# Optimization experiments

Measured on AMD Instinct MI355X. Metric: run time of the kernel, lower is better.

## Reference

```python
import jax, jax.numpy as jnp
import numpy as np

R = 16      # grid resolution per axis (G = R**3 voxels)
K = 8       # num KNN neighbors per voxel
H = 64      # num_hidden
NB = 2      # num conv blocks
EPS = 1e-5


def _conv3d(x, w, b):
    # x: [B,C,D,H,W], w: [O,I,3,3,3]
    y = jax.lax.conv_general_dilated(
        x, w, window_strides=(1, 1, 1), padding='SAME',
        dimension_numbers=('NCDHW', 'OIDHW', 'NCDHW'))
    return y + b[None, :, None, None, None]


def _bn(x):
    # training-mode BatchNorm3d statistics (no affine), per channel
    m = x.mean(axis=(0, 2, 3, 4), keepdims=True)
    v = x.var(axis=(0, 2, 3, 4), keepdims=True)
    return (x - m) * jax.lax.rsqrt(v + EPS)


def _forward(pos, x, pe_w1, pe_b1, pe_w2, pe_b2, f_w, f_b, up_w, up_b,
             conv_w, conv_b, on_g, on_b, ro_w, ro_b):
    B, N, _ = pos.shape
    # ---- Gridifier: coordinate grid over domain [-1, 1]^3 ----
    g1 = jnp.linspace(-1.0, 1.0, R, dtype=pos.dtype)
    grid = jnp.stack(jnp.meshgrid(g1, g1, g1, indexing='ij'), axis=-1).reshape(-1, 3)  # [G,3]
    # ---- brute-force KNN: points -> grid voxels (per graph) ----
    gn = jnp.sum(grid * grid, axis=-1)          # [G]
    pn = jnp.sum(pos * pos, axis=-1)            # [B,N]
    d = gn[None, :, None] + pn[:, None, :] - 2.0 * jnp.einsum('gc,bnc->bgn', grid, pos)  # [B,G,N]
    idx = jax.lax.top_k(jax.lax.stop_gradient(-d), K)[1]  # [B,G,K] nearest point indices
    b_ix = jnp.arange(B)[:, None, None]
    p_nb = pos[b_ix, idx]                       # [B,G,K,3] neighbor positions
    f_nb = x[b_ix, idx]                         # [B,G,K,Cin] neighbor features
    # ---- BipartiteConv: position-conditioned messages, mean aggregation ----
    rel = p_nb - grid[None, :, None, :]         # relative positions [B,G,K,3]
    pe = jax.nn.gelu(rel @ pe_w1 + pe_b1) @ pe_w2 + pe_b2   # position embed [B,G,K,H]
    msg = pe * (f_nb @ f_w + f_b)               # multiplicative conditioning [B,G,K,H]
    agg = msg.mean(axis=2)                      # [B,G,H]
    h = jax.nn.gelu(agg @ up_w + up_b)          # update net [B,G,H]
    # reshape(B,R,R,R,H).permute(0,4,3,2,1) -> NCDHW
    vol = h.reshape(B, R, R, R, H).transpose(0, 4, 3, 2, 1)  # [B,H,R,R,R]
    # ---- ConvNet3D: residual blocks, maxpool after block 0 ----
    for i in range(NB):
        h1 = jax.nn.relu(_bn(_conv3d(vol, conv_w[i, 0], conv_b[i, 0])))
        h2 = _bn(_conv3d(h1, conv_w[i, 1], conv_b[i, 1]))
        vol = jax.nn.relu(vol + h2)
        if i == 0:
            vol = jax.lax.reduce_window(vol, -jnp.inf, jax.lax.max,
                                        (1, 1, 2, 2, 2), (1, 1, 2, 2, 2), 'VALID')
    out = _bn(vol) * on_g[None, :, None, None, None] + on_b[None, :, None, None, None]
    # ---- mean readout pool + linear head ----
    pooled = out.mean(axis=(2, 3, 4))           # [B,H]
    return pooled @ ro_w + ro_b                 # [B,out_channels]


def setup_inputs() -> dict:
    key = jax.random.key(0)
    ks = jax.random.split(key, 10)
    B, N, Cin, OUT = 4, 4096, 3, 16
    s = 0.05
    return {
        'pos': jax.random.uniform(ks[0], (B, N, 3), jnp.float32, -1.0, 1.0),
        'x': jax.random.normal(ks[1], (B, N, Cin), jnp.float32),
        'pe_w1': jax.random.normal(ks[2], (3, H), jnp.float32) * 0.3,
        'pe_b1': jnp.zeros((H,), jnp.float32),
        'pe_w2': jax.random.normal(ks[3], (H, H), jnp.float32) * s,
        'pe_b2': jnp.zeros((H,), jnp.float32),
        'f_w': jax.random.normal(ks[4], (Cin, H), jnp.float32) * 0.3,
        'f_b': jnp.zeros((H,), jnp.float32),
        'up_w': jax.random.normal(ks[5], (H, H), jnp.float32) * s,
        'up_b': jnp.zeros((H,), jnp.float32),
        'conv_w': jax.random.normal(ks[6], (NB, 2, H, H, 3, 3, 3), jnp.float32) * s,
        'conv_b': jnp.zeros((NB, 2, H), jnp.float32),
        'on_g': jnp.ones((H,), jnp.float32),
        'on_b': jnp.zeros((H,), jnp.float32),
        'ro_w': jax.random.normal(ks[7], (H, OUT), jnp.float32) * s,
        'ro_b': jnp.zeros((OUT,), jnp.float32),
    }


def reference(pos, x, pe_w1, pe_b1, pe_w2, pe_b2, f_w, f_b, up_w, up_b,
              conv_w, conv_b, on_g, on_b, ro_w, ro_b):
    return _forward(pos, x, pe_w1, pe_b1, pe_w2, pe_b2, f_w, f_b, up_w, up_b,
                    conv_w, conv_b, on_g, on_b, ro_w, ro_b)
```

## Files before the change

kernel.cpp:

```cpp
#include <hip/hip_runtime.h>

#define ULL unsigned long long
typedef unsigned short ush;
typedef __attribute__((ext_vector_type(8))) short s8v;
typedef __attribute__((ext_vector_type(4))) float f4v;

#define BB 4
#define NP 4096
#define HH 64
#define EPSF 1e-5f

#define WH_OFF      0u
#define WL_OFF      221184u
#define WT_PER_CONV 110592u
#define IDX_OFF     442368u
#define VOL0_OFF    573440u
#define V0H_OFF     2066432u
#define V0L_OFF     2812928u
#define T1_OFF      3559424u
#define VOL1_OFF    4608000u
#define V1H_OFF     4864000u
#define V1L_OFF     4992000u
#define T3_OFF      5120000u
#define STATS_OFF   5251072u
#define CELLS_OFF   5251968u
#define SPOS_OFF    5268368u
#define MW_OFF      5333904u

#define ZN_V0   373248u
#define ZN_V1   64000u
#define ZN_ST   224u
#define ZN_ALL  (ZN_V0 + ZN_V1 + ZN_ST)

__device__ __forceinline__ ush f2bf(float f) {
  unsigned u = __float_as_uint(f);
  return (ush)((u + 0x7FFFu + ((u >> 16) & 1u)) >> 16);
}
__device__ __forceinline__ float bf2f(ush h) { return __uint_as_float(((unsigned)h) << 16); }

__device__ __forceinline__ float gelu_tanh(float v) {
  float inner = 0.7978845608028654f * (v + 0.044715f * v * v * v);
  return 0.5f * v * (1.0f + tanhf(inner));
}

__device__ __forceinline__ float lin16(int i) {
  return -1.0f + (float)i * (2.0f / 15.0f);
}

__global__ __launch_bounds__(256) void k_prep(const float* __restrict__ cw,
                                              const float* __restrict__ pw2,
                                              const float* __restrict__ upw,
                                              ush* __restrict__ wh,
                                              ush* __restrict__ wl,
                                              ush* __restrict__ mw,
                                              float* __restrict__ ws) {
  unsigned i = blockIdx.x * 256u + threadIdx.x;
  float4 z = make_float4(0.f, 0.f, 0.f, 0.f);
  if (i < ZN_V0) ((float4*)(ws + V0H_OFF))[i] = z;
  else if (i < ZN_V0 + ZN_V1) ((float4*)(ws + V1H_OFF))[i - ZN_V0] = z;
  else if (i < ZN_ALL) ((float4*)(ws + STATS_OFF))[i - ZN_V0 - ZN_V1] = z;
  if (i < 442368u) {
    unsigned conv = i / WT_PER_CONV;
    unsigned r = i - conv * WT_PER_CONV;
    unsigned co = r / 1728u;
    unsigned r2 = r - co * 1728u;
    unsigned ci = r2 / 27u;
    unsigned off = r2 - ci * 27u;
    float w = cw[i];
    ush hi = f2bf(w);
    unsigned dst = conv * WT_PER_CONV + (off * 64u + co) * 64u + ci;
    wh[dst] = hi;
    wl[dst] = f2bf(w - bf2f(hi));
  } else if (i < 450560u) {
    unsigned t = i - 442368u;
    unsigned mat = t >> 12, r = t & 4095u;
    unsigned co = r >> 6, ci = r & 63u;
    const float* src = mat ? upw : pw2;
    float w = src[ci * 64u + co];
    ush hi = f2bf(w);
    mw[mat * 8192u + co * 64u + ci] = hi;
    mw[mat * 8192u + 4096u + co * 64u + ci] = f2bf(w - bf2f(hi));
  }
}

__global__ __launch_bounds__(256) void k_bin(const float* __restrict__ pos,
                                             int* __restrict__ cellStart,
                                             float4* __restrict__ sortedPos) {
  __shared__ int cnt[4096];
  __shared__ int wsum[4];
  int tid = threadIdx.x;
  int b = blockIdx.x;
  const float* pb = pos + b * NP * 3;
  for (int i = tid; i < 4096; i += 256) cnt[i] = 0;
  __syncthreads();
#pragma unroll
  for (int t = 0; t < 16; ++t) {
    int p = t * 256 + tid;
    float px = pb[3 * p], py = pb[3 * p + 1], pz = pb[3 * p + 2];
    int c0 = (int)floorf((px + 1.0f) * 7.5f + 0.5f);
    int c1 = (int)floorf((py + 1.0f) * 7.5f + 0.5f);
    int c2 = (int)floorf((pz + 1.0f) * 7.5f + 0.5f);
    c0 = min(max(c0, 0), 15); c1 = min(max(c1, 0), 15); c2 = min(max(c2, 0), 15);
    atomicAdd(&cnt[(c0 * 16 + c1) * 16 + c2], 1);
  }
  __syncthreads();
  int base = tid * 16;
  int loc[16];
  int run = 0;
#pragma unroll
  for (int j = 0; j < 16; ++j) { loc[j] = run; run += cnt[base + j]; }
  int lane = tid & 63, wv = tid >> 6;
  int inc = run;
  for (int d = 1; d < 64; d <<= 1) {
    int o = __shfl_up(inc, d, 64);
    if (lane >= d) inc += o;
  }
  if (lane == 63) wsum[wv] = inc;
  __syncthreads();
  int woff = 0;
  for (int w = 0; w < wv; ++w) woff += wsum[w];
  int excl = woff + inc - run;
  __syncthreads();
  int stv[16];
#pragma unroll
  for (int j = 0; j < 16; ++j) {
    stv[j] = excl + loc[j];
    cellStart[b * 4097 + base + j] = stv[j];
  }
#pragma unroll
  for (int j = 0; j < 16; ++j) cnt[base + j] = stv[j];
  if (tid == 0) cellStart[b * 4097 + 4096] = NP;
  __syncthreads();
#pragma unroll
  for (int t = 0; t < 16; ++t) {
    int p = t * 256 + tid;
    float px = pb[3 * p], py = pb[3 * p + 1], pz = pb[3 * p + 2];
    int c0 = (int)floorf((px + 1.0f) * 7.5f + 0.5f);
    int c1 = (int)floorf((py + 1.0f) * 7.5f + 0.5f);
    int c2 = (int)floorf((pz + 1.0f) * 7.5f + 0.5f);
    c0 = min(max(c0, 0), 15); c1 = min(max(c1, 0), 15); c2 = min(max(c2, 0), 15);
    int slot = atomicAdd(&cnt[(c0 * 16 + c1) * 16 + c2], 1);
    sortedPos[b * 4096 + slot] = make_float4(px, py, pz, __int_as_float(p));
  }
}

__device__ __forceinline__ void ins8(ULL* kk, ULL key) {
  if (key < kk[7]) {
    kk[7] = key;
#pragma unroll
    for (int q = 7; q >= 1; --q) {
      ULL a = kk[q - 1], c = kk[q];
      bool sw = c < a;
      kk[q - 1] = sw ? c : a;
      kk[q] = sw ? a : c;
    }
  }
}
__device__ __forceinline__ ULL merge32(ULL* kk, int sub) {
  ULL win = ~0ULL;
#pragma unroll
  for (int r = 0; r < 8; ++r) {
    ULL m = kk[0];
#pragma unroll
    for (int s = 1; s < 32; s <<= 1) {
      ULL o = __shfl_xor(m, s, 64);
      m = (o < m) ? o : m;
    }
    if (kk[0] == m) {
#pragma unroll
      for (int q = 0; q < 7; ++q) kk[q] = kk[q + 1];
      kk[7] = ~0ULL;
    }
    if (sub == r) win = m;
  }
  return win;
}

__device__ __forceinline__ ULL mkkey(float4 c, float gx, float gy, float gz, float gn) {
  float pn = c.x * c.x + c.y * c.y + c.z * c.z;
  float dt = gx * c.x + gy * c.y + gz * c.z;
  float d = (gn + pn) - 2.0f * dt;
  unsigned u = __float_as_uint(d);
  u ^= (unsigned)((int)u >> 31) | 0x80000000u;
  return ((ULL)u << 32) | (unsigned)__float_as_uint(c.w);
}

__device__ __forceinline__ void scan_cell(const int* __restrict__ cs,
                                          const float4* __restrict__ sp,
                                          int cell, float gx, float gy, float gz,
                                          float gn, ULL* kk) {
  int st = cs[cell], en = cs[cell + 1];
  for (int p = st; p < en; ++p) ins8(kk, mkkey(sp[p], gx, gy, gz, gn));
}

__global__ __launch_bounds__(256) void k_knn5(const int* __restrict__ cellStart,
                                              const float4* __restrict__ sortedPos,
                                              int* __restrict__ idxo) {
  constexpr int CAP = 1024;
  __shared__ float4 pts[CAP];
  __shared__ int rst[64], rlen[64], rof[64];
  __shared__ int Tsh;
  int tid = threadIdx.x;
  int lane = tid & 63;
  int sub = tid & 31;
  int lv = tid >> 5;
  int blk = blockIdx.x;
  int b = blk >> 9;
  int t9 = blk & 511;
  int ii0 = (t9 >> 6) * 2, jj0 = ((t9 >> 3) & 7) * 2, kk0 = (t9 & 7) * 2;
  int ii = ii0 + (lv >> 2), jj = jj0 + ((lv >> 1) & 1), kkc = kk0 + (lv & 1);
  int g = (ii << 8) | (jj << 4) | kkc;
  float gx = lin16(ii), gy = lin16(jj), gz = lin16(kkc);
  float gn = gx * gx + gy * gy + gz * gz;
  const int* cs = cellStart + b * 4097;
  const float4* sp = sortedPos + b * 4096;
  int loa = max(ii0 - 3, 0), hia = min(ii0 + 4, 15);
  int lob = max(jj0 - 3, 0), hib = min(jj0 + 4, 15);
  int loc = max(kk0 - 3, 0), hic = min(kk0 + 4, 15);
  int Ra = hia - loa + 1, Rb = hib - lob + 1;
  int nrows = Ra * Rb;
  if (tid < 64) {
    int st = 0, len = 0;
    if (tid < nrows) {
      int a = loa + tid / Rb, c1 = lob + tid % Rb;
      int base = (a * 16 + c1) * 16;
      st = cs[base + loc];
      len = cs[base + hic + 1] - st;
    }
    rst[tid] = st;
    rlen[tid] = len;
    int s0 = len;
    for (int d = 1; d < 64; d <<= 1) { int o = __shfl_up(s0, d, 64); if (lane >= d) s0 += o; }
    rof[tid] = s0 - len;
    if (tid == 63) Tsh = s0;
  }
  __syncthreads();
  int T = Tsh;
  if (T <= CAP) {
    for (int i = tid; i < T; i += 256) {
// ... 129 lines not shown
      for (int n = 0; n < 4; ++n) {
        acc[m][n] = __builtin_amdgcn_mfma_f32_16x16x32_bf16(Ah, BH[n * 2 + ks], acc[m][n], 0, 0, 0);
        acc[m][n] = __builtin_amdgcn_mfma_f32_16x16x32_bf16(Ah, BL[n * 2 + ks], acc[m][n], 0, 0, 0);
        acc[m][n] = __builtin_amdgcn_mfma_f32_16x16x32_bf16(Al, BH[n * 2 + ks], acc[m][n], 0, 0, 0);
      }
    }
  float b2c[4];
#pragma unroll
  for (int n = 0; n < 4; ++n) b2c[n] = b2v[n * 16 + lm];
#pragma unroll
  for (int m = 0; m < 2; ++m) {
    int vox = wv * 4 + m * 2 + (quad >> 1);
#pragma unroll
    for (int n = 0; n < 4; ++n) {
      float s = 0.0f;
#pragma unroll
      for (int r = 0; r < 4; ++r) {
        int pair = wv * 32 + m * 16 + quad * 4 + r;
        s += (acc[m][n][r] + b2c[n]) * lfe[pair * 68 + n * 16 + lm];
      }
      s += __shfl_xor(s, 16, 64);
      s *= 0.125f;
      if ((quad & 1) == 0) {
        ush hi = f2bf(s);
        agH[vox * 72 + n * 16 + lm] = hi;
        agL[vox * 72 + n * 16 + lm] = f2bf(s - bf2f(hi));
      }
    }
  }
  __syncthreads();
  f4v a2 = (f4v){0.f, 0.f, 0.f, 0.f};
#pragma unroll
  for (int ks = 0; ks < 2; ++ks) {
    int ao = lm * 72 + ks * 32 + quad * 8;
    s8v Ah = *(const s8v*)&agH[ao];
    s8v Al = *(const s8v*)&agL[ao];
    a2 = __builtin_amdgcn_mfma_f32_16x16x32_bf16(Ah, UH[ks], a2, 0, 0, 0);
    a2 = __builtin_amdgcn_mfma_f32_16x16x32_bf16(Ah, UL[ks], a2, 0, 0, 0);
    a2 = __builtin_amdgcn_mfma_f32_16x16x32_bf16(Al, UH[ks], a2, 0, 0, 0);
  }
  int xc = g0 >> 8, yc = (g0 >> 4) & 15;
#pragma unroll
  for (int r = 0; r < 4; ++r) {
    int vox = quad * 4 + r;
    float h = gelu_tanh(a2[r] + ubc);
    int pidx = (((b * 18 + vox + 1) * 18 + yc + 1) * 18 + xc + 1) * 64 + wv * 16 + lm;
    vol0[pidx] = h;
    ush hi = f2bf(h);
    v0h[pidx] = hi;
    v0l[pidx] = f2bf(h - bf2f(hi));
  }
}

template <int Z>
__global__ __launch_bounds__(256) void k_convm(const ush* __restrict__ vh,
                                               const ush* __restrict__ vl,
                                               const ush* __restrict__ wh,
                                               const ush* __restrict__ wl,
                                               float* __restrict__ out,
                                               float* __restrict__ stats) {
  constexpr int P = Z + 2;
  constexpr int Py = (Z == 16) ? 6 : 10;
  constexpr int Px = (Z == 16) ? 18 : 10;
  constexpr int NV = 3 * Py * Px;
  constexpr int VS = 272;
  __shared__ unsigned char slab[NV * VS];
  __shared__ float ls[64], ls2[64];
  int tid = threadIdx.x;
  int lane = tid & 63, wv = tid >> 6;
  int vbase = blockIdx.x * 64;
  int b = (Z == 16) ? (vbase >> 12) : (vbase >> 9);
  int rem = vbase & (Z * Z * Z - 1);
  int z0 = rem / (Z * Z);
  int y0 = (Z == 16) ? ((rem & 255) >> 4) : 0;
  if (tid < 64) { ls[tid] = 0.0f; ls2[tid] = 0.0f; }
  {
    constexpr int NCH = NV * 8;
    for (int i = tid; i < NCH; i += 256) {
      int v = i >> 3, c = i & 7;
      int lz = v / (Py * Px);
      int r = v - lz * (Py * Px);
      int ly = r / Px, lx = r - ly * Px;
      int g = (((b * P + z0 + lz) * P + (y0 + ly)) * P + lx) * 64 + c * 8;
      *(uint4*)(slab + v * VS + c * 16)       = *(const uint4*)(vh + g);
      *(uint4*)(slab + v * VS + 128 + c * 16) = *(const uint4*)(vl + g);
    }
  }
  __syncthreads();
  int lm = lane & 15, quad = lane >> 4;
  int co = (wv << 4) | lm;
  f4v acc[4];
#pragma unroll
  for (int m = 0; m < 4; ++m) acc[m] = (f4v){0.f, 0.f, 0.f, 0.f};
  for (int off = 0; off < 27; ++off) {
    int dz = off / 9, r9 = off - dz * 9, dy = r9 / 3, dx = r9 - dy * 3;
    const ush* bph = wh + ((off * 64 + co) << 6) + (quad << 3);
    const ush* bpl = wl + ((off * 64 + co) << 6) + (quad << 3);
#pragma unroll
    for (int ks = 0; ks < 2; ++ks) {
      s8v bhf = *(const s8v*)(bph + ks * 32);
      s8v blf = *(const s8v*)(bpl + ks * 32);
#pragma unroll
      for (int m = 0; m < 4; ++m) {
        int lyp, lxp;
        if (Z == 16) { lyp = m + dy; lxp = lm + dx; }
        else         { lyp = 2 * m + (lm >> 3) + dy; lxp = (lm & 7) + dx; }
        int sv = (dz * Py + lyp) * Px + lxp;
        const unsigned char* ap = slab + sv * VS + (quad << 4) + (ks << 6);
        s8v ahf = *(const s8v*)(ap);
        s8v alf = *(const s8v*)(ap + 128);
        acc[m] = __builtin_amdgcn_mfma_f32_16x16x32_bf16(ahf, bhf, acc[m], 0, 0, 0);
        acc[m] = __builtin_amdgcn_mfma_f32_16x16x32_bf16(ahf, blf, acc[m], 0, 0, 0);
        acc[m] = __builtin_amdgcn_mfma_f32_16x16x32_bf16(alf, bhf, acc[m], 0, 0, 0);
      }
    }
  }
  float s = 0.0f, s2 = 0.0f;
#pragma unroll
  for (int m = 0; m < 4; ++m) {
    int vx = vbase + (m << 4) + (quad << 2);
#pragma unroll
    for (int r = 0; r < 4; ++r) {
      float v = acc[m][r];
      out[(vx + r) * 64 + co] = v;
      s += v;
      s2 = fmaf(v, v, s2);
    }
  }
  atomicAdd(&ls[co], s);
  atomicAdd(&ls2[co], s2);
  __syncthreads();
  if (tid < 64) {
    atomicAdd(&stats[tid * 2], ls[tid]);
    atomicAdd(&stats[tid * 2 + 1], ls2[tid]);
  }
}

template <int Z>
__global__ __launch_bounds__(256) void k_bnrelu(const float* __restrict__ t,
                                                const float* __restrict__ stats,
                                                ush* __restrict__ outh,
                                                ush* __restrict__ outl,
                                                float inv_cnt) {
  constexpr int P = Z + 2;
  unsigned i = blockIdx.x * 256u + threadIdx.x;
  int c = i & 63;
  int vox = i >> 6;
  int x = vox % Z;
  int q = vox / Z;
  int y = q % Z;
  q /= Z;
  int z = q % Z;
  int b = q / Z;
  float m = stats[c * 2] * inv_cnt;
  float var = stats[c * 2 + 1] * inv_cnt - m * m;
  float rs = 1.0f / sqrtf(var + EPSF);
  float v = (t[i] - m) * rs;
  v = v > 0.0f ? v : 0.0f;
  int pidx = (((b * P + z + 1) * P + y + 1) * P + x + 1) * 64 + c;
  ush hi = f2bf(v);
  outh[pidx] = hi;
  outl[pidx] = f2bf(v - bf2f(hi));
}

__global__ __launch_bounds__(256) void k_residpool(const float* __restrict__ vol0,
                                                   const float* __restrict__ t2,
                                                   const float* __restrict__ stats,
                                                   float* __restrict__ vol1,
                                                   ush* __restrict__ v1h,
                                                   ush* __restrict__ v1l) {
  unsigned i = blockIdx.x * 256u + threadIdx.x;
  int c = i & 63;
  int pv = i >> 6;
  int xp = pv & 7, yp = (pv >> 3) & 7, zp = (pv >> 6) & 7, b = pv >> 9;
  float m = stats[c * 2] * (1.0f / 16384.0f);
  float var = stats[c * 2 + 1] * (1.0f / 16384.0f) - m * m;
  float rs = 1.0f / sqrtf(var + EPSF);
  float best = 0.0f;
  for (int dz = 0; dz < 2; ++dz)
    for (int dy = 0; dy < 2; ++dy)
      for (int dx = 0; dx < 2; ++dx) {
        int z = 2 * zp + dz, y = 2 * yp + dy, x = 2 * xp + dx;
        float a = vol0[(((b * 18 + z + 1) * 18 + y + 1) * 18 + x + 1) * 64 + c];
        float t = t2[(b * 4096 + z * 256 + y * 16 + x) * 64 + c];
        float u = a + (t - m) * rs;
        u = u > 0.0f ? u : 0.0f;
        best = u > best ? u : best;
      }
  int pidx = (((b * 10 + zp + 1) * 10 + yp + 1) * 10 + xp + 1) * 64 + c;
  vol1[pidx] = best;
  ush hi = f2bf(best);
  v1h[pidx] = hi;
  v1l[pidx] = f2bf(best - bf2f(hi));
}

__global__ __launch_bounds__(256) void k_resid2(const float* __restrict__ vol1,
                                                const float* __restrict__ t4,
                                                const float* __restrict__ stats,
                                                float* __restrict__ sF,
                                                float* __restrict__ sB) {
  __shared__ float ls[64], ls2[64];
  if (threadIdx.x < 64) { ls[threadIdx.x] = 0.0f; ls2[threadIdx.x] = 0.0f; }
  __syncthreads();
  unsigned i = blockIdx.x * 256u + threadIdx.x;
  int c = i & 63;
  int pv = i >> 6;
  int x = pv & 7, y = (pv >> 3) & 7, z = (pv >> 6) & 7, b = pv >> 9;
  float m = stats[c * 2] * (1.0f / 2048.0f);
  float var = stats[c * 2 + 1] * (1.0f / 2048.0f) - m * m;
  float rs = 1.0f / sqrtf(var + EPSF);
  float a = vol1[(((b * 10 + z + 1) * 10 + y + 1) * 10 + x + 1) * 64 + c];
  float u = a + (t4[i] - m) * rs;
  u = u > 0.0f ? u : 0.0f;
  atomicAdd(&ls[c], u);
  atomicAdd(&ls2[c], u * u);
// ... 6 lines not shown
  }
}

__global__ __launch_bounds__(64) void k_final(const float* __restrict__ sF,
                                              const float* __restrict__ sB,
                                              const float* __restrict__ ong,
                                              const float* __restrict__ onb,
                                              const float* __restrict__ row,
                                              const float* __restrict__ rob,
                                              float* __restrict__ outp) {
  __shared__ float pl[4][64];
  int c = threadIdx.x;
  float m = sF[c * 2] * (1.0f / 2048.0f);
  float var = sF[c * 2 + 1] * (1.0f / 2048.0f) - m * m;
  float rs = 1.0f / sqrtf(var + EPSF);
  float gg = ong[c], bb = onb[c];
  for (int b = 0; b < 4; ++b)
    pl[b][c] = (sB[b * 64 + c] * (1.0f / 512.0f) - m) * rs * gg + bb;
  __syncthreads();
  int b = threadIdx.x >> 4, o = threadIdx.x & 15;
  float s = rob[o];
  for (int j = 0; j < 64; ++j) s = fmaf(pl[b][j], row[j * 16 + o], s);
  outp[b * 16 + o] = s;
}

extern "C" void kernel_launch(void* const* d_in, const int* in_sizes, int n_in,
                              void* d_out, int out_size, void* d_ws, size_t ws_size,
                              hipStream_t stream) {
  (void)in_sizes; (void)n_in; (void)out_size; (void)ws_size;
  const float* pos = (const float*)d_in[0];
  const float* xf  = (const float*)d_in[1];
  const float* pw1 = (const float*)d_in[2];
  const float* pb1 = (const float*)d_in[3];
  const float* pw2 = (const float*)d_in[4];
  const float* pb2 = (const float*)d_in[5];
  const float* fw  = (const float*)d_in[6];
  const float* fb  = (const float*)d_in[7];
  const float* uw  = (const float*)d_in[8];
  const float* ubp = (const float*)d_in[9];
  const float* cw  = (const float*)d_in[10];
  const float* ong = (const float*)d_in[12];
  const float* onb = (const float*)d_in[13];
  const float* row = (const float*)d_in[14];
  const float* rob = (const float*)d_in[15];

  float* ws   = (float*)d_ws;
  ush*   wh   = (ush*)(ws + WH_OFF);
  ush*   wl   = (ush*)(ws + WL_OFF);
  int*   idx  = (int*)(ws + IDX_OFF);
  float* vol0 = ws + VOL0_OFF;
  ush*   v0h  = (ush*)(ws + V0H_OFF);
  ush*   v0l  = (ush*)(ws + V0L_OFF);
  float* t1   = ws + T1_OFF;
  float* vol1 = ws + VOL1_OFF;
  ush*   v1h  = (ush*)(ws + V1H_OFF);
  ush*   v1l  = (ush*)(ws + V1L_OFF);
  float* t3   = ws + T3_OFF;
  float* sA   = ws + STATS_OFF;
  float* sF   = sA + 512;
  float* sB   = sF + 128;
  int*   cellStart = (int*)(ws + CELLS_OFF);
  float4* sortedPos = (float4*)(ws + SPOS_OFF);
  ush*   mw   = (ush*)(ws + MW_OFF);

  k_prep<<<1760, 256, 0, stream>>>(cw, pw2, uw, wh, wl, mw, ws);
  k_bin<<<4, 256, 0, stream>>>(pos, cellStart, sortedPos);
  k_knn5<<<2048, 256, 0, stream>>>(cellStart, sortedPos, idx);
  k_mlp2<<<1024, 256, 0, stream>>>(pos, xf, pw1, pb1, pb2, fw, fb, ubp,
                                   mw, mw + 4096, mw + 8192, mw + 12288,
                                   idx, vol0, v0h, v0l);
  k_convm<16><<<256, 256, 0, stream>>>(v0h, v0l, wh, wl, t1, sA);
  k_bnrelu<16><<<4096, 256, 0, stream>>>(t1, sA, v0h, v0l, 1.0f / 16384.0f);
  k_convm<16><<<256, 256, 0, stream>>>(v0h, v0l, wh + WT_PER_CONV, wl + WT_PER_CONV,
                                       t1, sA + 128);
  k_residpool<<<512, 256, 0, stream>>>(vol0, t1, sA + 128, vol1, v1h, v1l);
  k_convm<8><<<32, 256, 0, stream>>>(v1h, v1l, wh + 2 * WT_PER_CONV,
                                     wl + 2 * WT_PER_CONV, t3, sA + 256);
  k_bnrelu<8><<<512, 256, 0, stream>>>(t3, sA + 256, v1h, v1l, 1.0f / 2048.0f);
  k_convm<8><<<32, 256, 0, stream>>>(v1h, v1l, wh + 3 * WT_PER_CONV,
                                     wl + 3 * WT_PER_CONV, t3, sA + 384);
  k_resid2<<<512, 256, 0, stream>>>(vol1, t3, sA + 384, sF, sB);
  k_final<<<1, 64, 0, stream>>>(sF, sB, ong, onb, row, rob, (float*)d_out);
}
```

Measured before the change: 300.1 us.

## Merge prep and binning kernels; halve conv tile to double block count

Folds the weight-prep/zeroing kernel and the point-binning kernel into one launch, with the first four blocks doing binning and the rest doing prep. The 3D conv kernel now gives each block 32 output voxels instead of 64, with a smaller input slab, so the conv launches use twice as many blocks and fill more CUs on the small grids. The cost is more redundant halo loads per output and more atomic stat reductions.

Result: slower. 336.5 us (+12.1%).

```diff
diff --git a/kernel.cpp b/kernel.cpp
--- a/kernel.cpp
+++ b/kernel.cpp
@@ -47,100 +47,101 @@
   return -1.0f + (float)i * (2.0f / 15.0f);
 }
 
-__global__ __launch_bounds__(256) void k_prep(const float* __restrict__ cw,
-                                              const float* __restrict__ pw2,
-                                              const float* __restrict__ upw,
-                                              ush* __restrict__ wh,
-                                              ush* __restrict__ wl,
-                                              ush* __restrict__ mw,
-                                              float* __restrict__ ws) {
-  unsigned i = blockIdx.x * 256u + threadIdx.x;
-  float4 z = make_float4(0.f, 0.f, 0.f, 0.f);
-  if (i < ZN_V0) ((float4*)(ws + V0H_OFF))[i] = z;
-  else if (i < ZN_V0 + ZN_V1) ((float4*)(ws + V1H_OFF))[i - ZN_V0] = z;
-  else if (i < ZN_ALL) ((float4*)(ws + STATS_OFF))[i - ZN_V0 - ZN_V1] = z;
-  if (i < 442368u) {
-    unsigned conv = i / WT_PER_CONV;
-    unsigned r = i - conv * WT_PER_CONV;
-    unsigned co = r / 1728u;
-    unsigned r2 = r - co * 1728u;
-    unsigned ci = r2 / 27u;
-    unsigned off = r2 - ci * 27u;
-    float w = cw[i];
-    ush hi = f2bf(w);
-    unsigned dst = conv * WT_PER_CONV + (off * 64u + co) * 64u + ci;
-    wh[dst] = hi;
-    wl[dst] = f2bf(w - bf2f(hi));
-  } else if (i < 450560u) {
-    unsigned t = i - 442368u;
-    unsigned mat = t >> 12, r = t & 4095u;
-    unsigned co = r >> 6, ci = r & 63u;
-    const float* src = mat ? upw : pw2;
-    float w = src[ci * 64u + co];
-    ush hi = f2bf(w);
-    mw[mat * 8192u + co * 64u + ci] = hi;
-    mw[mat * 8192u + 4096u + co * 64u + ci] = f2bf(w - bf2f(hi));
-  }
-}
-
-__global__ __launch_bounds__(256) void k_bin(const float* __restrict__ pos,
-                                             int* __restrict__ cellStart,
-                                             float4* __restrict__ sortedPos) {
+__global__ __launch_bounds__(256) void k_prepbin(const float* __restrict__ cw,
+                                                 const float* __restrict__ pw2,
+                                                 const float* __restrict__ upw,
+                                                 const float* __restrict__ pos,
+                                                 ush* __restrict__ wh,
+                                                 ush* __restrict__ wl,
+                                                 ush* __restrict__ mw,
+                                                 float* __restrict__ ws,
+                                                 int* __restrict__ cellStart,
+                                                 float4* __restrict__ sortedPos) {
   __shared__ int cnt[4096];
   __shared__ int wsum[4];
   int tid = threadIdx.x;
-  int b = blockIdx.x;
-  const float* pb = pos + b * NP * 3;
-  for (int i = tid; i < 4096; i += 256) cnt[i] = 0;
-  __syncthreads();
-#pragma unroll
-  for (int t = 0; t < 16; ++t) {
-    int p = t * 256 + tid;
-    float px = pb[3 * p], py = pb[3 * p + 1], pz = pb[3 * p + 2];
-    int c0 = (int)floorf((px + 1.0f) * 7.5f + 0.5f);
-    int c1 = (int)floorf((py + 1.0f) * 7.5f + 0.5f);
-    int c2 = (int)floorf((pz + 1.0f) * 7.5f + 0.5f);
-    c0 = min(max(c0, 0), 15); c1 = min(max(c1, 0), 15); c2 = min(max(c2, 0), 15);
-    atomicAdd(&cnt[(c0 * 16 + c1) * 16 + c2], 1);
-  }
-  __syncthreads();
-  int base = tid * 16;
-  int loc[16];
-  int run = 0;
-#pragma unroll
-  for (int j = 0; j < 16; ++j) { loc[j] = run; run += cnt[base + j]; }
-  int lane = tid & 63, wv = tid >> 6;
-  int inc = run;
-  for (int d = 1; d < 64; d <<= 1) {
-    int o = __shfl_up(inc, d, 64);
-    if (lane >= d) inc += o;
-  }
-  if (lane == 63) wsum[wv] = inc;
-  __syncthreads();
-  int woff = 0;
-  for (int w = 0; w < wv; ++w) woff += wsum[w];
-  int excl = woff + inc - run;
-  __syncthreads();
-  int stv[16];
-#pragma unroll
-  for (int j = 0; j < 16; ++j) {
-    stv[j] = excl + loc[j];
-    cellStart[b * 4097 + base + j] = stv[j];
-  }
-#pragma unroll
-  for (int j = 0; j < 16; ++j) cnt[base + j] = stv[j];
-  if (tid == 0) cellStart[b * 4097 + 4096] = NP;
-  __syncthreads();
-#pragma unroll
-  for (int t = 0; t < 16; ++t) {
-    int p = t * 256 + tid;
-    float px = pb[3 * p], py = pb[3 * p + 1], pz = pb[3 * p + 2];
-    int c0 = (int)floorf((px + 1.0f) * 7.5f + 0.5f);
-    int c1 = (int)floorf((py + 1.0f) * 7.5f + 0.5f);
-    int c2 = (int)floorf((pz + 1.0f) * 7.5f + 0.5f);
-    c0 = min(max(c0, 0), 15); c1 = min(max(c1, 0), 15); c2 = min(max(c2, 0), 15);
-    int slot = atomicAdd(&cnt[(c0 * 16 + c1) * 16 + c2], 1);
-    sortedPos[b * 4096 + slot] = make_float4(px, py, pz, __int_as_float(p));
+  if (blockIdx.x < 4) {
+    int b = blockIdx.x;
+    const float* pb = pos + b * NP * 3;
+    for (int i = tid; i < 4096; i += 256) cnt[i] = 0;
+    __syncthreads();
+#pragma unroll
+    for (int t = 0; t < 16; ++t) {
+      int p = t * 256 + tid;
+      float px = pb[3 * p], py = pb[3 * p + 1], pz = pb[3 * p + 2];
+      int c0 = (int)floorf((px + 1.0f) * 7.5f + 0.5f);
+      int c1 = (int)floorf((py + 1.0f) * 7.5f + 0.5f);
+      int c2 = (int)floorf((pz + 1.0f) * 7.5f + 0.5f);
+      c0 = min(max(c0, 0), 15); c1 = min(max(c1, 0), 15); c2 = min(max(c2, 0), 15);
+      atomicAdd(&cnt[(c0 * 16 + c1) * 16 + c2], 1);
+    }
+    __syncthreads();
+    int base = tid * 16;
+    int loc[16];
+    int run = 0;
+#pragma unroll
+    for (int j = 0; j < 16; ++j) { loc[j] = run; run += cnt[base + j]; }
+    int lane = tid & 63, wv = tid >> 6;
+    int inc = run;
+    for (int d = 1; d < 64; d <<= 1) {
+      int o = __shfl_up(inc, d, 64);
+      if (lane >= d) inc += o;
+    }
+    if (lane == 63) wsum[wv] = inc;
+    __syncthreads();
+    int woff = 0;
+    for (int w = 0; w < wv; ++w) woff += wsum[w];
+    int excl = woff + inc - run;
+    __syncthreads();
+    int stv[16];
+#pragma unroll
+    for (int j = 0; j < 16; ++j) {
+      stv[j] = excl + loc[j];
+      cellStart[b * 4097 + base + j] = stv[j];
+    }
+#pragma unroll
+    for (int j = 0; j < 16; ++j) cnt[base + j] = stv[j];
+    if (tid == 0) cellStart[b * 4097 + 4096] = NP;
+    __syncthreads();
+#pragma unroll
+    for (int t = 0; t < 16; ++t) {
+      int p = t * 256 + tid;
+      float px = pb[3 * p], py = pb[3 * p + 1], pz = pb[3 * p + 2];
+      int c0 = (int)floorf((px + 1.0f) * 7.5f + 0.5f);
+      int c1 = (int)floorf((py + 1.0f) * 7.5f + 0.5f);
+      int c2 = (int)floorf((pz + 1.0f) * 7.5f + 0.5f);
+      c0 = min(max(c0, 0), 15); c1 = min(max(c1, 0), 15); c2 = min(max(c2, 0), 15);
+      int slot = atomicAdd(&cnt[(c0 * 16 + c1) * 16 + c2], 1);
+      sortedPos[b * 4096 + slot] = make_float4(px, py, pz, __int_as_float(p));
+    }
+  } else {
+    unsigned i = (blockIdx.x - 4) * 256u + tid;
+    float4 z = make_float4(0.f, 0.f, 0.f, 0.f);
+    if (i < ZN_V0) ((float4*)(ws + V0H_OFF))[i] = z;
+    else if (i < ZN_V0 + ZN_V1) ((float4*)(ws + V1H_OFF))[i - ZN_V0] = z;
+    else if (i < ZN_ALL) ((float4*)(ws + STATS_OFF))[i - ZN_V0 - ZN_V1] = z;
+    if (i < 442368u) {
+      unsigned conv = i / WT_PER_CONV;
+      unsigned r = i - conv * WT_PER_CONV;
+      unsigned co = r / 1728u;
+      unsigned r2 = r - co * 1728u;
+      unsigned ci = r2 / 27u;
+      unsigned off = r2 - ci * 27u;
+      float w = cw[i];
+      ush hi = f2bf(w);
+      unsigned dst = conv * WT_PER_CONV + (off * 64u + co) * 64u + ci;
+      wh[dst] = hi;
+      wl[dst] = f2bf(w - bf2f(hi));
+    } else if (i < 450560u) {
+      unsigned t = i - 442368u;
+      unsigned mat = t >> 12, r = t & 4095u;
+      unsigned co = r >> 6, ci = r & 63u;
+      const float* src = mat ? upw : pw2;
+      float w = src[ci * 64u + co];
+      ush hi = f2bf(w);
+      mw[mat * 8192u + co * 64u + ci] = hi;
+      mw[mat * 8192u + 4096u + co * 64u + ci] = f2bf(w - bf2f(hi));
+    }
   }
 }
 
@@ -175,7 +176,6 @@
   }
   return win;
 }
-
 __device__ __forceinline__ ULL mkkey(float4 c, float gx, float gy, float gz, float gn) {
   float pn = c.x * c.x + c.y * c.y + c.z * c.z;
   float dt = gx * c.x + gy * c.y + gz * c.z;
@@ -184,7 +184,6 @@
   u ^= (unsigned)((int)u >> 31) | 0x80000000u;
   return ((ULL)u << 32) | (unsigned)__float_as_uint(c.w);
 }
-
 __device__ __forceinline__ void scan_cell(const int* __restrict__ cs,
                                           const float4* __restrict__ sp,
                                           int cell, float gx, float gy, float gz,
@@ -421,14 +420,14 @@
 }
 
 template <int Z>
-__global__ __launch_bounds__(256) void k_convm(const ush* __restrict__ vh,
-                                               const ush* __restrict__ vl,
-                                               const ush* __restrict__ wh,
-                                               const ush* __restrict__ wl,
-                                               float* __restrict__ out,
-                                               float* __restrict__ stats) {
+__global__ __launch_bounds__(256) void k_conv32(const ush* __restrict__ vh,
+                                                const ush* __restrict__ vl,
+                                                const ush* __restrict__ wtH,
+                                                const ush* __restrict__ wtL,
+                                                float* __restrict__ out,
+                                                float* __restrict__ stats) {
   constexpr int P = Z + 2;
-  constexpr int Py = (Z == 16) ? 6 : 10;
+  constexpr int Py = (Z == 16) ? 4 : 6;
   constexpr int Px = (Z == 16) ? 18 : 10;
   constexpr int NV = 3 * Py * Px;
   constexpr int VS = 272;
@@ -436,44 +435,41 @@
   __shared__ float ls[64], ls2[64];
   int tid = threadIdx.x;
   int lane = tid & 63, wv = tid >> 6;
-  int vbase = blockIdx.x * 64;
-  int b = (Z == 16) ? (vbase >> 12) : (vbase >> 9);
-  int rem = vbase & (Z * Z * Z - 1);
-  int z0 = rem / (Z * Z);
-  int y0 = (Z == 16) ? ((rem & 255) >> 4) : 0;
+  int bb = blockIdx.x;
+  int vbase = bb * 32;
+  int b, z, y0;
+  if (Z == 16) { b = vbase >> 12; int rem = vbase & 4095; z = rem >> 8; y0 = (rem >> 4) & 15; }
+  else         { b = vbase >> 9;  int rem = vbase & 511;  z = rem >> 6; y0 = (rem >> 3) & 7; }
   if (tid < 64) { ls[tid] = 0.0f; ls2[tid] = 0.0f; }
-  {
-    constexpr int NCH = NV * 8;
-    for (int i = tid; i < NCH; i += 256) {
-      int v = i >> 3, c = i & 7;
-      int lz = v / (Py * Px);
-      int r = v - lz * (Py * Px);
-      int ly = r / Px, lx = r - ly * Px;
-      int g = (((b * P + z0 + lz) * P + (y0 + ly)) * P + lx) * 64 + c * 8;
-      *(uint4*)(slab + v * VS + c * 16)       = *(const uint4*)(vh + g);
-      *(uint4*)(slab + v * VS + 128 + c * 16) = *(const uint4*)(vl + g);
-    }
+  for (int i = tid; i < NV * 8; i += 256) {
+    int v = i >> 3, c = i & 7;
+    int lz = v / (Py * Px);
+    int r = v - lz * (Py * Px);
+    int ly = r / Px, lx = r - ly * Px;
+    int g = (((b * P + (z + lz)) * P + (y0 + ly)) * P + lx) * 64 + c * 8;
+    *(uint4*)(slab + v * VS + c * 16)       = *(const uint4*)(vh + g);
+    *(uint4*)(slab + v * VS + 128 + c * 16) = *(const uint4*)(vl + g);
   }
   __syncthreads();
   int lm = lane & 15, quad = lane >> 4;
   int co = (wv << 4) | lm;
-  f4v acc[4];
-#pragma unroll
-  for (int m = 0; m < 4; ++m) acc[m] = (f4v){0.f, 0.f, 0.f, 0.f};
+  f4v acc[2];
+  acc[0] = (f4v){0.f, 0.f, 0.f, 0.f};
+  acc[1] = (f4v){0.f, 0.f, 0.f, 0.f};
   for (int off = 0; off < 27; ++off) {
     int dz = off / 9, r9 = off - dz * 9, dy = r9 / 3, dx = r9 - dy * 3;
-    const ush* bph = wh + ((off * 64 + co) << 6) + (quad << 3);
-    const ush* bpl = wl + ((off * 64 + co) << 6) + (quad << 3);
+    const ush* bph = wtH + ((off * 64 + co) << 6) + (quad << 3);
+    const ush* bpl = wtL + ((off * 64 + co) << 6) + (quad << 3);
 #pragma unroll
     for (int ks = 0; ks < 2; ++ks) {
       s8v bhf = *(const s8v*)(bph + ks * 32);
       s8v blf = *(const s8v*)(bpl + ks * 32);
 #pragma unroll
-      for (int m = 0; m < 4; ++m) {
-        int lyp, lxp;
-        if (Z == 16) { lyp = m + dy; lxp = lm + dx; }
-        else         { lyp = 2 * m + (lm >> 3) + dy; lxp = (lm & 7) + dx; }
-        int sv = (dz * Py + lyp) * Px + lxp;
+      for (int m = 0; m < 2; ++m) {
+        int ly2, lx2;
+        if (Z == 16) { ly2 = m + dy; lx2 = lm + dx; }
+        else         { ly2 = m * 2 + (lm >> 3) + dy; lx2 = (lm & 7) + dx; }
+        int sv = (dz * Py + ly2) * Px + lx2;
         const unsigned char* ap = slab + sv * VS + (quad << 4) + (ks << 6);
         s8v ahf = *(const s8v*)(ap);
         s8v alf = *(const s8v*)(ap + 128);
@@ -485,7 +481,7 @@
   }
   float s = 0.0f, s2 = 0.0f;
 #pragma unroll
-  for (int m = 0; m < 4; ++m) {
+  for (int m = 0; m < 2; ++m) {
     int vx = vbase + (m << 4) + (quad << 2);
 #pragma unroll
     for (int r = 0; r < 4; ++r) {
@@ -652,22 +648,22 @@
   float4* sortedPos = (float4*)(ws + SPOS_OFF);
   ush*   mw   = (ush*)(ws + MW_OFF);
 
-  k_prep<<<1760, 256, 0, stream>>>(cw, pw2, uw, wh, wl, mw, ws);
-  k_bin<<<4, 256, 0, stream>>>(pos, cellStart, sortedPos);
+  k_prepbin<<<1764, 256, 0, stream>>>(cw, pw2, uw, pos, wh, wl, mw, ws,
+                                      cellStart, sortedPos);
   k_knn5<<<2048, 256, 0, stream>>>(cellStart, sortedPos, idx);
   k_mlp2<<<1024, 256, 0, stream>>>(pos, xf, pw1, pb1, pb2, fw, fb, ubp,
                                    mw, mw + 4096, mw + 8192, mw + 12288,
                                    idx, vol0, v0h, v0l);
-  k_convm<16><<<256, 256, 0, stream>>>(v0h, v0l, wh, wl, t1, sA);
+  k_conv32<16><<<512, 256, 0, stream>>>(v0h, v0l, wh, wl, t1, sA);
   k_bnrelu<16><<<4096, 256, 0, stream>>>(t1, sA, v0h, v0l, 1.0f / 16384.0f);
-  k_convm<16><<<256, 256, 0, stream>>>(v0h, v0l, wh + WT_PER_CONV, wl + WT_PER_CONV,
-                                       t1, sA + 128);
+  k_conv32<16><<<512, 256, 0, stream>>>(v0h, v0l, wh + WT_PER_CONV, wl + WT_PER_CONV,
+                                        t1, sA + 128);
   k_residpool<<<512, 256, 0, stream>>>(vol0, t1, sA + 128, vol1, v1h, v1l);
-  k_convm<8><<<32, 256, 0, stream>>>(v1h, v1l, wh + 2 * WT_PER_CONV,
-                                     wl + 2 * WT_PER_CONV, t3, sA + 256);
+  k_conv32<8><<<64, 256, 0, stream>>>(v1h, v1l, wh + 2 * WT_PER_CONV,
+                                      wl + 2 * WT_PER_CONV, t3, sA + 256);
   k_bnrelu<8><<<512, 256, 0, stream>>>(t3, sA + 256, v1h, v1l, 1.0f / 2048.0f);
-  k_convm<8><<<32, 256, 0, stream>>>(v1h, v1l, wh + 3 * WT_PER_CONV,
-                                     wl + 3 * WT_PER_CONV, t3, sA + 384);
+  k_conv32<8><<<64, 256, 0, stream>>>(v1h, v1l, wh + 3 * WT_PER_CONV,
+                                      wl + 3 * WT_PER_CONV, t3, sA + 384);
   k_resid2<<<512, 256, 0, stream>>>(vol1, t3, sA + 384, sF, sB);
   k_final<<<1, 64, 0, stream>>>(sF, sB, ong, onb, row, rob, (float*)d_out);
 }
```

## Fuse BN+ReLU into conv input staging, merge prep/bin, prefetch conv weights

Applied to the files above, without the earlier changes.

The separate batchnorm+ReLU kernels are removed. The second conv of each block now reads the raw fp32 conv output, normalizes it, applies ReLU, and splits it to bf16 hi/lo while staging its input slab. The weight-prep and point-binning kernels are merged into one launch, and conv weight fragments are loaded one kernel-offset ahead in registers. These changes save launches and a round trip through memory, at the cost of more registers and reusing workspace regions as outputs of the second conv.

Result: no change. 294.9 us, median of 2 (-1.7%).

```diff
diff --git a/kernel.cpp b/kernel.cpp
--- a/kernel.cpp
+++ b/kernel.cpp
@@ -47,100 +47,101 @@
   return -1.0f + (float)i * (2.0f / 15.0f);
 }
 
-__global__ __launch_bounds__(256) void k_prep(const float* __restrict__ cw,
-                                              const float* __restrict__ pw2,
-                                              const float* __restrict__ upw,
-                                              ush* __restrict__ wh,
-                                              ush* __restrict__ wl,
-                                              ush* __restrict__ mw,
-                                              float* __restrict__ ws) {
-  unsigned i = blockIdx.x * 256u + threadIdx.x;
-  float4 z = make_float4(0.f, 0.f, 0.f, 0.f);
-  if (i < ZN_V0) ((float4*)(ws + V0H_OFF))[i] = z;
-  else if (i < ZN_V0 + ZN_V1) ((float4*)(ws + V1H_OFF))[i - ZN_V0] = z;
-  else if (i < ZN_ALL) ((float4*)(ws + STATS_OFF))[i - ZN_V0 - ZN_V1] = z;
-  if (i < 442368u) {
-    unsigned conv = i / WT_PER_CONV;
-    unsigned r = i - conv * WT_PER_CONV;
-    unsigned co = r / 1728u;
-    unsigned r2 = r - co * 1728u;
-    unsigned ci = r2 / 27u;
-    unsigned off = r2 - ci * 27u;
-    float w = cw[i];
-    ush hi = f2bf(w);
-    unsigned dst = conv * WT_PER_CONV + (off * 64u + co) * 64u + ci;
-    wh[dst] = hi;
-    wl[dst] = f2bf(w - bf2f(hi));
-  } else if (i < 450560u) {
-    unsigned t = i - 442368u;
-    unsigned mat = t >> 12, r = t & 4095u;
-    unsigned co = r >> 6, ci = r & 63u;
-    const float* src = mat ? upw : pw2;
-    float w = src[ci * 64u + co];
-    ush hi = f2bf(w);
-    mw[mat * 8192u + co * 64u + ci] = hi;
-    mw[mat * 8192u + 4096u + co * 64u + ci] = f2bf(w - bf2f(hi));
-  }
-}
-
-__global__ __launch_bounds__(256) void k_bin(const float* __restrict__ pos,
-                                             int* __restrict__ cellStart,
-                                             float4* __restrict__ sortedPos) {
+__global__ __launch_bounds__(256) void k_prepbin(const float* __restrict__ cw,
+                                                 const float* __restrict__ pw2,
+                                                 const float* __restrict__ upw,
+                                                 const float* __restrict__ pos,
+                                                 ush* __restrict__ wh,
+                                                 ush* __restrict__ wl,
+                                                 ush* __restrict__ mw,
+                                                 float* __restrict__ ws,
+                                                 int* __restrict__ cellStart,
+                                                 float4* __restrict__ sortedPos) {
   __shared__ int cnt[4096];
   __shared__ int wsum[4];
   int tid = threadIdx.x;
-  int b = blockIdx.x;
-  const float* pb = pos + b * NP * 3;
-  for (int i = tid; i < 4096; i += 256) cnt[i] = 0;
-  __syncthreads();
-#pragma unroll
-  for (int t = 0; t < 16; ++t) {
-    int p = t * 256 + tid;
-    float px = pb[3 * p], py = pb[3 * p + 1], pz = pb[3 * p + 2];
-    int c0 = (int)floorf((px + 1.0f) * 7.5f + 0.5f);
-    int c1 = (int)floorf((py + 1.0f) * 7.5f + 0.5f);
-    int c2 = (int)floorf((pz + 1.0f) * 7.5f + 0.5f);
-    c0 = min(max(c0, 0), 15); c1 = min(max(c1, 0), 15); c2 = min(max(c2, 0), 15);
-    atomicAdd(&cnt[(c0 * 16 + c1) * 16 + c2], 1);
-  }
-  __syncthreads();
-  int base = tid * 16;
-  int loc[16];
-  int run = 0;
-#pragma unroll
-  for (int j = 0; j < 16; ++j) { loc[j] = run; run += cnt[base + j]; }
-  int lane = tid & 63, wv = tid >> 6;
-  int inc = run;
-  for (int d = 1; d < 64; d <<= 1) {
-    int o = __shfl_up(inc, d, 64);
-    if (lane >= d) inc += o;
-  }
-  if (lane == 63) wsum[wv] = inc;
-  __syncthreads();
-  int woff = 0;
-  for (int w = 0; w < wv; ++w) woff += wsum[w];
-  int excl = woff + inc - run;
-  __syncthreads();
-  int stv[16];
-#pragma unroll
-  for (int j = 0; j < 16; ++j) {
-    stv[j] = excl + loc[j];
-    cellStart[b * 4097 + base + j] = stv[j];
-  }
-#pragma unroll
-  for (int j = 0; j < 16; ++j) cnt[base + j] = stv[j];
-  if (tid == 0) cellStart[b * 4097 + 4096] = NP;
-  __syncthreads();
-#pragma unroll
-  for (int t = 0; t < 16; ++t) {
-    int p = t * 256 + tid;
-    float px = pb[3 * p], py = pb[3 * p + 1], pz = pb[3 * p + 2];
-    int c0 = (int)floorf((px + 1.0f) * 7.5f + 0.5f);
-    int c1 = (int)floorf((py + 1.0f) * 7.5f + 0.5f);
-    int c2 = (int)floorf((pz + 1.0f) * 7.5f + 0.5f);
-    c0 = min(max(c0, 0), 15); c1 = min(max(c1, 0), 15); c2 = min(max(c2, 0), 15);
-    int slot = atomicAdd(&cnt[(c0 * 16 + c1) * 16 + c2], 1);
-    sortedPos[b * 4096 + slot] = make_float4(px, py, pz, __int_as_float(p));
+  if (blockIdx.x < 4) {
+    int b = blockIdx.x;
+    const float* pb = pos + b * NP * 3;
+    for (int i = tid; i < 4096; i += 256) cnt[i] = 0;
+    __syncthreads();
+#pragma unroll
+    for (int t = 0; t < 16; ++t) {
+      int p = t * 256 + tid;
+      float px = pb[3 * p], py = pb[3 * p + 1], pz = pb[3 * p + 2];
+      int c0 = (int)floorf((px + 1.0f) * 7.5f + 0.5f);
+      int c1 = (int)floorf((py + 1.0f) * 7.5f + 0.5f);
+      int c2 = (int)floorf((pz + 1.0f) * 7.5f + 0.5f);
+      c0 = min(max(c0, 0), 15); c1 = min(max(c1, 0), 15); c2 = min(max(c2, 0), 15);
+      atomicAdd(&cnt[(c0 * 16 + c1) * 16 + c2], 1);
+    }
+    __syncthreads();
+    int base = tid * 16;
+    int loc[16];
+    int run = 0;
+#pragma unroll
+    for (int j = 0; j < 16; ++j) { loc[j] = run; run += cnt[base + j]; }
+    int lane = tid & 63, wv = tid >> 6;
+    int inc = run;
+    for (int d = 1; d < 64; d <<= 1) {
+      int o = __shfl_up(inc, d, 64);
+      if (lane >= d) inc += o;
+    }
+    if (lane == 63) wsum[wv] = inc;
+    __syncthreads();
+    int woff = 0;
+    for (int w = 0; w < wv; ++w) woff += wsum[w];
+    int excl = woff + inc - run;
+    __syncthreads();
+    int stv[16];
+#pragma unroll
+    for (int j = 0; j < 16; ++j) {
+      stv[j] = excl + loc[j];
+      cellStart[b * 4097 + base + j] = stv[j];
+    }
+#pragma unroll
+    for (int j = 0; j < 16; ++j) cnt[base + j] = stv[j];
+    if (tid == 0) cellStart[b * 4097 + 4096] = NP;
+    __syncthreads();
+#pragma unroll
+    for (int t = 0; t < 16; ++t) {
+      int p = t * 256 + tid;
+      float px = pb[3 * p], py = pb[3 * p + 1], pz = pb[3 * p + 2];
+      int c0 = (int)floorf((px + 1.0f) * 7.5f + 0.5f);
+      int c1 = (int)floorf((py + 1.0f) * 7.5f + 0.5f);
+      int c2 = (int)floorf((pz + 1.0f) * 7.5f + 0.5f);
+      c0 = min(max(c0, 0), 15); c1 = min(max(c1, 0), 15); c2 = min(max(c2, 0), 15);
+      int slot = atomicAdd(&cnt[(c0 * 16 + c1) * 16 + c2], 1);
+      sortedPos[b * 4096 + slot] = make_float4(px, py, pz, __int_as_float(p));
+    }
+  } else {
+    unsigned i = (blockIdx.x - 4) * 256u + tid;
+    float4 z = make_float4(0.f, 0.f, 0.f, 0.f);
+    if (i < ZN_V0) ((float4*)(ws + V0H_OFF))[i] = z;
+    else if (i < ZN_V0 + ZN_V1) ((float4*)(ws + V1H_OFF))[i - ZN_V0] = z;
+    else if (i < ZN_ALL) ((float4*)(ws + STATS_OFF))[i - ZN_V0 - ZN_V1] = z;
+    if (i < 442368u) {
+      unsigned conv = i / WT_PER_CONV;
+      unsigned r = i - conv * WT_PER_CONV;
+      unsigned co = r / 1728u;
+      unsigned r2 = r - co * 1728u;
+      unsigned ci = r2 / 27u;
+      unsigned off = r2 - ci * 27u;
+      float w = cw[i];
+      ush hi = f2bf(w);
+      unsigned dst = conv * WT_PER_CONV + (off * 64u + co) * 64u + ci;
+      wh[dst] = hi;
+      wl[dst] = f2bf(w - bf2f(hi));
+    } else if (i < 450560u) {
+      unsigned t = i - 442368u;
+      unsigned mat = t >> 12, r = t & 4095u;
+      unsigned co = r >> 6, ci = r & 63u;
+      const float* src = mat ? upw : pw2;
+      float w = src[ci * 64u + co];
+      ush hi = f2bf(w);
+      mw[mat * 8192u + co * 64u + ci] = hi;
+      mw[mat * 8192u + 4096u + co * 64u + ci] = f2bf(w - bf2f(hi));
+    }
   }
 }
 
@@ -175,7 +176,6 @@
   }
   return win;
 }
-
 __device__ __forceinline__ ULL mkkey(float4 c, float gx, float gy, float gz, float gn) {
   float pn = c.x * c.x + c.y * c.y + c.z * c.z;
   float dt = gx * c.x + gy * c.y + gz * c.z;
@@ -184,7 +184,6 @@
   u ^= (unsigned)((int)u >> 31) | 0x80000000u;
   return ((ULL)u << 32) | (unsigned)__float_as_uint(c.w);
 }
-
 __device__ __forceinline__ void scan_cell(const int* __restrict__ cs,
                                           const float4* __restrict__ sp,
                                           int cell, float gx, float gy, float gz,
@@ -420,11 +419,14 @@
   }
 }
 
-template <int Z>
+template <int Z, int FUSED>
 __global__ __launch_bounds__(256) void k_convm(const ush* __restrict__ vh,
                                                const ush* __restrict__ vl,
-                                               const ush* __restrict__ wh,
-                                               const ush* __restrict__ wl,
+                                               const float* __restrict__ tin,
+                                               const float* __restrict__ instats,
+                                               float inv_cnt,
+                                               const ush* __restrict__ wtH,
+                                               const ush* __restrict__ wtL,
                                                float* __restrict__ out,
                                                float* __restrict__ stats) {
   constexpr int P = Z + 2;
@@ -442,9 +444,50 @@
   int z0 = rem / (Z * Z);
   int y0 = (Z == 16) ? ((rem & 255) >> 4) : 0;
   if (tid < 64) { ls[tid] = 0.0f; ls2[tid] = 0.0f; }
-  {
-    constexpr int NCH = NV * 8;
-    for (int i = tid; i < NCH; i += 256) {
+  if (FUSED) {
+    float mreg[8], rreg[8];
+    int cb = (tid & 7) * 8;
+#pragma unroll
+    for (int e = 0; e < 8; ++e) {
+      float sm = instats[(cb + e) * 2];
+      float sq = instats[(cb + e) * 2 + 1];
+      float m = sm * inv_cnt;
+      float var = sq * inv_cnt - m * m;
+      mreg[e] = m;
+      rreg[e] = 1.0f / sqrtf(var + EPSF);
+    }
+    for (int i = tid; i < NV * 8; i += 256) {
+      int v = i >> 3, c = i & 7;
+      int lz = v / (Py * Px);
+      int r = v - lz * (Py * Px);
+      int ly = r / Px, lx = r - ly * Px;
+      int rz = z0 + lz - 1, ry = y0 + ly - 1, rx = lx - 1;
+      bool ok = ((unsigned)rz < (unsigned)Z) & ((unsigned)ry < (unsigned)Z) &
+                ((unsigned)rx < (unsigned)Z);
+      float vv[8];
+#pragma unroll
+      for (int e = 0; e < 8; ++e) vv[e] = 0.0f;
+      if (ok) {
+        const float* tp = tin + ((((b * Z + rz) * Z + ry) * Z + rx) << 6) + c * 8;
+        float4 f0 = *(const float4*)tp;
+        float4 f1 = *(const float4*)(tp + 4);
+        vv[0] = f0.x; vv[1] = f0.y; vv[2] = f0.z; vv[3] = f0.w;
+        vv[4] = f1.x; vv[5] = f1.y; vv[6] = f1.z; vv[7] = f1.w;
+      }
+      union { ush u[8]; uint4 q; } ph, pq;
+#pragma unroll
+      for (int e = 0; e < 8; ++e) {
+        float x = (vv[e] - mreg[e]) * rreg[e];
+        x = (ok && x > 0.0f) ? x : 0.0f;
+        ush h = f2bf(x);
+        ph.u[e] = h;
+        pq.u[e] = f2bf(x - bf2f(h));
+      }
+      *(uint4*)(slab + v * VS + c * 16) = ph.q;
+      *(uint4*)(slab + v * VS + 128 + c * 16) = pq.q;
+    }
+  } else {
+    for (int i = tid; i < NV * 8; i += 256) {
       int v = i >> 3, c = i & 7;
       int lz = v / (Py * Px);
       int r = v - lz * (Py * Px);
@@ -457,17 +500,24 @@
   __syncthreads();
   int lm = lane & 15, quad = lane >> 4;
   int co = (wv << 4) | lm;
+  const ush* bH = wtH + (co << 6) + (quad << 3);
+  const ush* bL = wtL + (co << 6) + (quad << 3);
+  s8v cH0 = *(const s8v*)(bH), cH1 = *(const s8v*)(bH + 32);
+  s8v cL0 = *(const s8v*)(bL), cL1 = *(const s8v*)(bL + 32);
   f4v acc[4];
 #pragma unroll
   for (int m = 0; m < 4; ++m) acc[m] = (f4v){0.f, 0.f, 0.f, 0.f};
   for (int off = 0; off < 27; ++off) {
+    int noff = (off < 26) ? off + 1 : 26;
+    const ush* nbH = bH + noff * 4096;
+    const ush* nbL = bL + noff * 4096;
+    s8v nH0 = *(const s8v*)(nbH), nH1 = *(const s8v*)(nbH + 32);
+    s8v nL0 = *(const s8v*)(nbL), nL1 = *(const s8v*)(nbL + 32);
     int dz = off / 9, r9 = off - dz * 9, dy = r9 / 3, dx = r9 - dy * 3;
-    const ush* bph = wh + ((off * 64 + co) << 6) + (quad << 3);
-    const ush* bpl = wl + ((off * 64 + co) << 6) + (quad << 3);
 #pragma unroll
     for (int ks = 0; ks < 2; ++ks) {
-      s8v bhf = *(const s8v*)(bph + ks * 32);
-      s8v blf = *(const s8v*)(bpl + ks * 32);
+      s8v bhf = ks ? cH1 : cH0;
+      s8v blf = ks ? cL1 : cL0;
 #pragma unroll
       for (int m = 0; m < 4; ++m) {
         int lyp, lxp;
@@ -482,6 +532,7 @@
         acc[m] = __builtin_amdgcn_mfma_f32_16x16x32_bf16(alf, bhf, acc[m], 0, 0, 0);
       }
     }
+    cH0 = nH0; cH1 = nH1; cL0 = nL0; cL1 = nL1;
   }
   float s = 0.0f, s2 = 0.0f;
 #pragma unroll
@@ -502,33 +553,6 @@
     atomicAdd(&stats[tid * 2], ls[tid]);
     atomicAdd(&stats[tid * 2 + 1], ls2[tid]);
   }
-}
-
-template <int Z>
-__global__ __launch_bounds__(256) void k_bnrelu(const float* __restrict__ t,
-                                                const float* __restrict__ stats,
-                                                ush* __restrict__ outh,
-                                                ush* __restrict__ outl,
-                                                float inv_cnt) {
-  constexpr int P = Z + 2;
-  unsigned i = blockIdx.x * 256u + threadIdx.x;
-  int c = i & 63;
-  int vox = i >> 6;
-  int x = vox % Z;
-  int q = vox / Z;
-  int y = q % Z;
-  q /= Z;
-  int z = q % Z;
-  int b = q / Z;
-  float m = stats[c * 2] * inv_cnt;
-  float var = stats[c * 2 + 1] * inv_cnt - m * m;
-  float rs = 1.0f / sqrtf(var + EPSF);
-  float v = (t[i] - m) * rs;
-  v = v > 0.0f ? v : 0.0f;
-  int pidx = (((b * P + z + 1) * P + y + 1) * P + x + 1) * 64 + c;
-  ush hi = f2bf(v);
-  outh[pidx] = hi;
-  outl[pidx] = f2bf(v - bf2f(hi));
 }
 
 __global__ __launch_bounds__(256) void k_residpool(const float* __restrict__ vol0,
@@ -641,10 +665,12 @@
   ush*   v0h  = (ush*)(ws + V0H_OFF);
   ush*   v0l  = (ush*)(ws + V0L_OFF);
   float* t1   = ws + T1_OFF;
+  float* t2   = ws + V0H_OFF;
   float* vol1 = ws + VOL1_OFF;
   ush*   v1h  = (ush*)(ws + V1H_OFF);
   ush*   v1l  = (ush*)(ws + V1L_OFF);
   float* t3   = ws + T3_OFF;
+  float* t4   = ws + V1H_OFF;
   float* sA   = ws + STATS_OFF;
   float* sF   = sA + 512;
   float* sB   = sF + 128;
@@ -652,22 +678,24 @@
   float4* sortedPos = (float4*)(ws + SPOS_OFF);
   ush*   mw   = (ush*)(ws + MW_OFF);
 
-  k_prep<<<1760, 256, 0, stream>>>(cw, pw2, uw, wh, wl, mw, ws);
-  k_bin<<<4, 256, 0, stream>>>(pos, cellStart, sortedPos);
+  k_prepbin<<<1764, 256, 0, stream>>>(cw, pw2, uw, pos, wh, wl, mw, ws,
+                                      cellStart, sortedPos);
   k_knn5<<<2048, 256, 0, stream>>>(cellStart, sortedPos, idx);
   k_mlp2<<<1024, 256, 0, stream>>>(pos, xf, pw1, pb1, pb2, fw, fb, ubp,
                                    mw, mw + 4096, mw + 8192, mw + 12288,
                                    idx, vol0, v0h, v0l);
-  k_convm<16><<<256, 256, 0, stream>>>(v0h, v0l, wh, wl, t1, sA);
-  k_bnrelu<16><<<4096, 256, 0, stream>>>(t1, sA, v0h, v0l, 1.0f / 16384.0f);
-  k_convm<16><<<256, 256, 0, stream>>>(v0h, v0l, wh + WT_PER_CONV, wl + WT_PER_CONV,
-                                       t1, sA + 128);
-  k_residpool<<<512, 256, 0, stream>>>(vol0, t1, sA + 128, vol1, v1h, v1l);
-  k_convm<8><<<32, 256, 0, stream>>>(v1h, v1l, wh + 2 * WT_PER_CONV,
-                                     wl + 2 * WT_PER_CONV, t3, sA + 256);
-  k_bnrelu<8><<<512, 256, 0, stream>>>(t3, sA + 256, v1h, v1l, 1.0f / 2048.0f);
-  k_convm<8><<<32, 256, 0, stream>>>(v1h, v1l, wh + 3 * WT_PER_CONV,
-                                     wl + 3 * WT_PER_CONV, t3, sA + 384);
-  k_resid2<<<512, 256, 0, stream>>>(vol1, t3, sA + 384, sF, sB);
+  k_convm<16, 0><<<256, 256, 0, stream>>>(v0h, v0l, nullptr, nullptr, 0.0f,
+                                          wh, wl, t1, sA);
+  k_convm<16, 1><<<256, 256, 0, stream>>>(nullptr, nullptr, t1, sA, 1.0f / 16384.0f,
+                                          wh + WT_PER_CONV, wl + WT_PER_CONV,
+                                          t2, sA + 128);
+  k_residpool<<<512, 256, 0, stream>>>(vol0, t2, sA + 128, vol1, v1h, v1l);
+  k_convm<8, 0><<<32, 256, 0, stream>>>(v1h, v1l, nullptr, nullptr, 0.0f,
+                                        wh + 2 * WT_PER_CONV, wl + 2 * WT_PER_CONV,
+                                        t3, sA + 256);
+  k_convm<8, 1><<<32, 256, 0, stream>>>(nullptr, nullptr, t3, sA + 256, 1.0f / 2048.0f,
+                                        wh + 3 * WT_PER_CONV, wl + 3 * WT_PER_CONV,
+                                        t4, sA + 384);
+  k_resid2<<<512, 256, 0, stream>>>(vol1, t4, sA + 384, sF, sB);
   k_final<<<1, 64, 0, stream>>>(sF, sB, ong, onb, row, rob, (float*)d_out);
 }
```
